# Kernel optimization log

Hardware: AMD Instinct MI355X
Metric: run time of the kernel (lower is better)

Reference implementation:

```python
import jax, jax.numpy as jnp
import numpy as np

N_NODES = 100000
N_EDGES = 3200000
IN_CH, HID, OUT_CH = 11, 64, 1


def setup_inputs() -> dict:
    key = jax.random.key(0)
    ks = jax.random.split(key, 10)
    x = jax.random.normal(ks[0], (N_NODES, IN_CH), dtype=jnp.float32)
    edge_index = jax.random.randint(ks[1], (2, N_EDGES), 0, N_NODES, dtype=jnp.int64)
    s = lambda k, shape, fan_in: jax.random.normal(k, shape, jnp.float32) * (1.0 / np.sqrt(fan_in))
    return {
        "x": x,
        "edge_index": edge_index,
        # conv1: lin_l acts on aggregated neighbors (has bias), lin_r on root (no bias)
        "Wl1": s(ks[2], (HID, IN_CH), IN_CH), "bl1": jnp.zeros((HID,), jnp.float32),
        "Wr1": s(ks[3], (HID, IN_CH), IN_CH),
        "Wl2": s(ks[4], (HID, HID), HID), "bl2": jnp.zeros((HID,), jnp.float32),
        "Wr2": s(ks[5], (HID, HID), HID),
        "Wlin": s(ks[6], (OUT_CH, HID), HID), "blin": jnp.zeros((OUT_CH,), jnp.float32),
    }


def _sage_conv(x, src, dst, Wl, bl, Wr):
    # mean aggregation of source features onto destination nodes
    msg = x[src]                                            # [E, d] gather
    agg = jax.ops.segment_sum(msg, dst, num_segments=N_NODES)          # [N, d]
    cnt = jax.ops.segment_sum(jnp.ones_like(dst, jnp.float32), dst, num_segments=N_NODES)
    mean = agg / jnp.maximum(cnt, 1.0)[:, None]             # isolated nodes -> 0
    return mean @ Wl.T + bl + x @ Wr.T


def reference(x, edge_index, Wl1, bl1, Wr1, Wl2, bl2, Wr2, Wlin, blin):
    src, dst = edge_index[0], edge_index[1]
    h = jax.nn.relu(_sage_conv(x, src, dst, Wl1, bl1, Wr1))
    h = jax.nn.relu(_sage_conv(h, src, dst, Wl2, bl2, Wr2))
    return h @ Wlin.T + blin
```

## Files before the change

kernel.cpp:

```cpp
#include <hip/hip_runtime.h>
#include <hip/hip_fp16.h>

#define IN_CH 11
#define HID 64
#define PAD 64
#define OVCAP 16384
#define NBLK 512
#define BSH 7
#define NBKT 782
#define CAP8 768

typedef _Float16 half8_t __attribute__((ext_vector_type(8)));
typedef float f32x4_t __attribute__((ext_vector_type(4)));

__global__ void k_prep(const float* __restrict__ x, const float* __restrict__ Wl2,
                       const float* __restrict__ Wr2, unsigned* __restrict__ xphu,
                       __half* __restrict__ wl2h, __half* __restrict__ wr2h,
                       int* __restrict__ ovcnt, int* __restrict__ bcnt8, int N) {
    int i = blockIdx.x * blockDim.x + threadIdx.x;
    if (i == 0) *ovcnt = 0;
    if (i < 8 * NBKT) bcnt8[i] = 0;
    if (i < HID * HID) {
        wl2h[i] = __float2half_rn(Wl2[i]);
        wr2h[i] = __float2half_rn(Wr2[i]);
    }
    if (i < (N + 1) * 8) {
        int n = i >> 3, j = (i & 7) * 2;
        float a = 0.f, b = 0.f;
        if (n < N) {
            if (j < IN_CH) a = x[n * IN_CH + j];
            if (j + 1 < IN_CH) b = x[n * IN_CH + j + 1];
        }
        unsigned lo = (unsigned)__half_as_ushort(__float2half_rn(a));
        unsigned hi = (unsigned)__half_as_ushort(__float2half_rn(b));
        xphu[i] = lo | (hi << 16);
    }
}

__global__ __launch_bounds__(256) void k_build(const int* __restrict__ src,
        const int* __restrict__ dst, unsigned* __restrict__ ebuf,
        int* __restrict__ bcnt8, int* __restrict__ ovcnt, int* __restrict__ ov,
        int E, int csz) {
    __shared__ int h[NBKT];
    __shared__ int cur[NBKT];
    __shared__ int lim[NBKT];
    int tid = threadIdx.x, blk = blockIdx.x;
    int xcd = blk & 7;
    for (int t = tid; t < NBKT; t += 256) h[t] = 0;
    __syncthreads();
    int c0 = blk * csz, c1 = min(c0 + csz, E);
    for (int base = c0; base < c1; base += 1024) {
        int d[4]; bool ok[4];
        #pragma unroll
        for (int k = 0; k < 4; k++) {
            int e = base + tid + k * 256;
            ok[k] = e < c1;
            d[k] = ok[k] ? dst[e] : 0;
        }
        #pragma unroll
        for (int k = 0; k < 4; k++)
            if (ok[k]) atomicAdd(&h[d[k] >> BSH], 1);
    }
    __syncthreads();
    for (int t = tid; t < NBKT; t += 256) {
        int hc = h[t];
        int cell = xcd * NBKT + t;
        int base = cell * CAP8;
        int off = (hc > 0) ? atomicAdd(&bcnt8[cell], hc) : 0;
        cur[t] = base + off;
        lim[t] = base + CAP8;
    }
    __syncthreads();
    for (int base = c0; base < c1; base += 1024) {
        int d[4], s[4], slot[4];
        bool ok[4];
        #pragma unroll
        for (int k = 0; k < 4; k++) {
            int e = base + tid + k * 256;
            ok[k] = e < c1;
            d[k] = ok[k] ? dst[e] : 0;
            s[k] = ok[k] ? __builtin_nontemporal_load(&src[e]) : 0;
        }
        #pragma unroll
        for (int k = 0; k < 4; k++)
            if (ok[k]) slot[k] = atomicAdd(&cur[d[k] >> BSH], 1);
        #pragma unroll
        for (int k = 0; k < 4; k++) {
            if (!ok[k]) continue;
            if (slot[k] < lim[d[k] >> BSH]) {
                ebuf[slot[k]] = ((unsigned)s[k] << 7) | (unsigned)(d[k] & 127);
            } else {
                int q = atomicAdd(ovcnt, 1);
                if (q < OVCAP) { ov[2 * q] = d[k]; ov[2 * q + 1] = s[k]; }
            }
        }
    }
}

__global__ __launch_bounds__(256) void k_bbuild(const unsigned* __restrict__ ebuf,
        const int* __restrict__ bcnt8,
        int* __restrict__ cnt, int* __restrict__ col64,
        int* __restrict__ ovcnt, int* __restrict__ ov, int N) {
    __shared__ int lc[128];
    __shared__ int colsh[128 * PAD];
    int tid = threadIdx.x, b = blockIdx.x;
    int lo = b << BSH, hi = min(lo + 128, N);
    #pragma unroll
    for (int i = 0; i < 8; i++)
        ((int4*)colsh)[tid + i * 256] = make_int4(N, N, N, N);
    if (tid < 128) lc[tid] = 0;
    __syncthreads();
    for (int x = 0; x < 8; x++) {
        int cell = x * NBKT + b;
        int cc = min(bcnt8[cell], CAP8);
        const unsigned* seg = ebuf + (size_t)cell * CAP8;
        for (int i = tid; i < cc; i += 256) {
            unsigned p = __builtin_nontemporal_load(&seg[i]);
            int row = (int)(p & 127u);
            int sv  = (int)(p >> 7);
            int r = atomicAdd(&lc[row], 1);
            if (r < PAD) {
                colsh[(row << 6) | r] = sv;
            } else {
                int q = atomicAdd(ovcnt, 1);
                if (q < OVCAP) { ov[2 * q] = lo + row; ov[2 * q + 1] = sv; }
            }
        }
    }
    __syncthreads();
    int nn = hi - lo;
    int4* dst4 = (int4*)col64 + (size_t)lo * 16;
    for (int i = tid; i < nn * 16; i += 256) dst4[i] = ((int4*)colsh)[i];
    if (tid < nn) cnt[lo + tid] = lc[tid];
}

__global__ void k_agg1(const unsigned* __restrict__ xphu,
                       const int* __restrict__ col64,
                       float* __restrict__ agg1, int N) {
    int lane = threadIdx.x & 63;
    int n = blockIdx.x * 4 + (threadIdx.x >> 6);
    if (n >= N) return;
    int c8 = lane & 7, sub = lane >> 3;
    const int* cb = col64 + n * PAD;
    int s[8];
    #pragma unroll
    for (int jj = 0; jj < 8; jj++) s[jj] = __builtin_nontemporal_load(&cb[sub + 8 * jj]);
    unsigned v[8];
    #pragma unroll
    for (int jj = 0; jj < 8; jj++) v[jj] = xphu[s[jj] * 8 + c8];
    __half2 a2 = __floats2half2_rn(0.f, 0.f);
    #pragma unroll
    for (int jj = 0; jj < 8; jj++) a2 = __hadd2(a2, *(__half2*)&v[jj]);
    float2 f = __half22float2(a2);
    #pragma unroll
    for (int off = 8; off <= 32; off <<= 1) {
        f.x += __shfl_xor(f.x, off);
        f.y += __shfl_xor(f.y, off);
    }
    if (lane < 8) ((float2*)agg1)[n * 8 + lane] = f;
}

__global__ void k_ov1(const int* __restrict__ ovcnt, const int* __restrict__ ov,
                      const float* __restrict__ x, float* __restrict__ agg1) {
    int c = *ovcnt; if (c > OVCAP) c = OVCAP;
    for (int i = blockIdx.x * blockDim.x + threadIdx.x; i < c;
         i += gridDim.x * blockDim.x) {
        int d = ov[2 * i], s = ov[2 * i + 1];
        for (int ch = 0; ch < IN_CH; ch++)
            atomicAdd(&agg1[d * 16 + ch], x[s * IN_CH + ch]);
    }
}

__global__ void k_dense1(const float* __restrict__ x, const float* __restrict__ agg1,
                         const int* __restrict__ cnt, const float* __restrict__ Wl,
                         const float* __restrict__ bl, const float* __restrict__ Wr,
                         unsigned* __restrict__ h1h, int N) {
    int lane = threadIdx.x & 63;
    int n = blockIdx.x * 4 + (threadIdx.x >> 6);
    if (n > N) return;
    if (n == N) {
        if (lane < 32) h1h[n * 32 + lane] = 0u;
        return;
    }
    int deg = cnt[n];
    float inv = deg > 0 ? 1.f / (float)deg : 0.f;
    float mv = (lane < 16) ? agg1[n * 16 + lane] * inv : 0.f;
    float xv = (lane < IN_CH) ? x[n * IN_CH + lane] : 0.f;
    float h = bl[lane];
    #pragma unroll
    for (int c = 0; c < IN_CH; c++)
        h += Wl[lane * IN_CH + c] * __shfl(mv, c) + Wr[lane * IN_CH + c] * __shfl(xv, c);
    h = fmaxf(h, 0.f);
    unsigned my = (unsigned)__half_as_ushort(__float2half_rn(h));
    unsigned nx = __shfl_down(my, 1);
    if ((lane & 1) == 0) h1h[n * 32 + (lane >> 1)] = my | (nx << 16);
}

__global__ void k_agg2(const uint4* __restrict__ h1h4, const int* __restrict__ col64,
                       const int* __restrict__ cnt, unsigned* __restrict__ agg2h,
                       int N) {
    int lane = threadIdx.x & 63;
    int n = blockIdx.x * 4 + (threadIdx.x >> 6);
    if (n >= N) return;
    int c8 = lane & 7, sub = lane >> 3;
    const int* cb = col64 + n * PAD;
    int s[8];
    #pragma unroll
    for (int jj = 0; jj < 8; jj++) s[jj] = __builtin_nontemporal_load(&cb[sub + 8 * jj]);
    uint4 v[8];
    #pragma unroll
    for (int jj = 0; jj < 8; jj++) v[jj] = h1h4[s[jj] * 8 + c8];
    __half2 a2[4];
    #pragma unroll
    for (int t = 0; t < 4; t++) a2[t] = __floats2half2_rn(0.f, 0.f);
    #pragma unroll
    for (int jj = 0; jj < 8; jj++) {
        a2[0] = __hadd2(a2[0], *(__half2*)&v[jj].x);
        a2[1] = __hadd2(a2[1], *(__half2*)&v[jj].y);
        a2[2] = __hadd2(a2[2], *(__half2*)&v[jj].z);
        a2[3] = __hadd2(a2[3], *(__half2*)&v[jj].w);
    }
    float acc[8];
    #pragma unroll
    for (int t = 0; t < 4; t++) {
        float2 f = __half22float2(a2[t]);
        acc[2 * t] = f.x; acc[2 * t + 1] = f.y;
    }
    #pragma unroll
    for (int off = 8; off <= 32; off <<= 1) {
        #pragma unroll
        for (int t = 0; t < 8; t++) acc[t] += __shfl_xor(acc[t], off);
    }
    if (sub == 0) {
        int deg = cnt[n];
        float inv = deg > 0 ? 1.f / (float)deg : 0.f;
        __half2 h0 = __floats2half2_rn(acc[0] * inv, acc[1] * inv);
        __half2 h1 = __floats2half2_rn(acc[2] * inv, acc[3] * inv);
        __half2 h2 = __floats2half2_rn(acc[4] * inv, acc[5] * inv);
        __half2 h3 = __floats2half2_rn(acc[6] * inv, acc[7] * inv);
        uint4 o;
        o.x = *(unsigned*)&h0; o.y = *(unsigned*)&h1;
        o.z = *(unsigned*)&h2; o.w = *(unsigned*)&h3;
        ((uint4*)agg2h)[n * 8 + c8] = o;
    }
}

__global__ void k_ov2(const int* __restrict__ ovcnt, const int* __restrict__ ov,
                      const unsigned* __restrict__ h1h, const int* __restrict__ cnt,
                      unsigned* __restrict__ agg2h) {
    int c = *ovcnt; if (c > OVCAP) c = OVCAP;
    for (int i = blockIdx.x * blockDim.x + threadIdx.x; i < c;
         i += gridDim.x * blockDim.x) {
        int d = ov[2 * i], s = ov[2 * i + 1];
        int deg = cnt[d];
        float inv = deg > 0 ? 1.f / (float)deg : 0.f;
        const __half2* hp = (const __half2*)(h1h + s * 32);
        __half2* ap = (__half2*)(agg2h + d * 32);
        for (int ch = 0; ch < 32; ch++) {
            float2 f = __half22float2(hp[ch]);
            __half2 adv = __floats2half2_rn(f.x * inv, f.y * inv);
            unsafeAtomicAdd(&ap[ch], adv);
        }
    }
}

__global__ __launch_bounds__(256) void k_dense2(
    const uint4* __restrict__ agg2h4, const uint4* __restrict__ h1h_u4,
    const __half* __restrict__ wl2h, const __half* __restrict__ wr2h,
    const float* __restrict__ bl, const float* __restrict__ Wlin,
    const float* __restrict__ blin, float* __restrict__ out, int N) {
    union U { uint4 u; half8_t h; };
    int lane = threadIdx.x & 63;
    int wave = blockIdx.x * 4 + (threadIdx.x >> 6);
    int nwaves = gridDim.x * 4;
    int r16 = lane & 15, quad = lane >> 4;
    const uint4* wlu = (const uint4*)wl2h;
    const uint4* wru = (const uint4*)wr2h;
    half8_t bfr[4][4];
    #pragma unroll
    for (int tt = 0; tt < 4; tt++) {
        int o = tt * 16 + r16;
        U t0, t1, t2, t3;
        t0.u = wlu[o * 8 + quad];
        t1.u = wlu[o * 8 + 4 + quad];
        t2.u = wru[o * 8 + quad];
        t3.u = wru[o * 8 + 4 + quad];
        bfr[tt][0] = t0.h; bfr[tt][1] = t1.h; bfr[tt][2] = t2.h; bfr[tt][3] = t3.h;
    }
    float bl_c[4], wl_c[4];
    #pragma unroll
    for (int tt = 0; tt < 4; tt++) {
        bl_c[tt] = bl[tt * 16 + r16];
        wl_c[tt] = Wlin[tt * 16 + r16];
    }
    float b0 = blin[0];
    int ntiles = (N + 15) >> 4;
    for (int t = wave; t < ntiles; t += nwaves) {
        int nb = t * 16;
        int n = nb + r16; if (n >= N) n = N - 1;
        U a0, a1, a2, a3;
        a0.u = agg2h4[n * 8 + quad];
        a1.u = agg2h4[n * 8 + 4 + quad];
        a2.u = h1h_u4[n * 8 + quad];
        a3.u = h1h_u4[n * 8 + 4 + quad];
        float p0 = 0.f, p1 = 0.f, p2 = 0.f, p3 = 0.f;
        #pragma unroll
        for (int tt = 0; tt < 4; tt++) {
            f32x4_t c = {0.f, 0.f, 0.f, 0.f};
            c = __builtin_amdgcn_mfma_f32_16x16x32_f16(a0.h, bfr[tt][0], c, 0, 0, 0);
            c = __builtin_amdgcn_mfma_f32_16x16x32_f16(a1.h, bfr[tt][1], c, 0, 0, 0);
            c = __builtin_amdgcn_mfma_f32_16x16x32_f16(a2.h, bfr[tt][2], c, 0, 0, 0);
            c = __builtin_amdgcn_mfma_f32_16x16x32_f16(a3.h, bfr[tt][3], c, 0, 0, 0);
            p0 += fmaxf(c[0] + bl_c[tt], 0.f) * wl_c[tt];
            p1 += fmaxf(c[1] + bl_c[tt], 0.f) * wl_c[tt];
            p2 += fmaxf(c[2] + bl_c[tt], 0.f) * wl_c[tt];
            p3 += fmaxf(c[3] + bl_c[tt], 0.f) * wl_c[tt];
        }
        #pragma unroll
        for (int off = 1; off <= 8; off <<= 1) {
            p0 += __shfl_xor(p0, off); p1 += __shfl_xor(p1, off);
            p2 += __shfl_xor(p2, off); p3 += __shfl_xor(p3, off);
        }
        if (r16 == 0) {
            int nn = nb + quad * 4;
            if (nn + 3 < N) {
                ((float4*)out)[nn >> 2] = make_float4(p0 + b0, p1 + b0, p2 + b0, p3 + b0);
            } else {
                if (nn + 0 < N) out[nn + 0] = p0 + b0;
                if (nn + 1 < N) out[nn + 1] = p1 + b0;
                if (nn + 2 < N) out[nn + 2] = p2 + b0;
                if (nn + 3 < N) out[nn + 3] = p3 + b0;
            }
        }
    }
}


extern "C" void kernel_launch(void* const* d_in, const int* in_sizes, int n_in,
                              void* d_out, int out_size, void* d_ws, size_t ws_size,
                              hipStream_t stream) {
    const float* x    = (const float*)d_in[0];
    const int*   ei   = (const int*)d_in[1];
    const float* Wl1  = (const float*)d_in[2];
    const float* bl1  = (const float*)d_in[3];
    const float* Wr1  = (const float*)d_in[4];
    const float* Wl2  = (const float*)d_in[5];
    const float* bl2  = (const float*)d_in[6];
    const float* Wr2  = (const float*)d_in[7];
    const float* Wlin = (const float*)d_in[8];
    const float* blin = (const float*)d_in[9];
    float* out = (float*)d_out;

    int N = in_sizes[0] / IN_CH;
    int E = in_sizes[1] / 2;
    const int* srcp = ei;
    const int* dstp = ei + E;

    int* ws       = (int*)d_ws;
    int* cnt      = ws;
    int* ovcnt    = ws + N;
    int* col64    = ws + 100032;
    unsigned* xph = (unsigned*)(ws + 6500032);
    unsigned* ebuf= (unsigned*)(ws + 7300064);
    int* bcnt8    = ws + 12104672;
    float* agg1   = (float*)(ws + 7300064);
    unsigned* agg2h = (unsigned*)(ws + 6500032);
    unsigned* h1h = (unsigned*)(ws + 12900096);
    int* ov       = ws + 16100128;
    __half* wl2h  = (__half*)(ws + 16132896);
    __half* wr2h  = (__half*)(ws + 16134944);

    int csz = (E + NBLK - 1) / NBLK;

    k_prep   <<<((N + 1) * 8 + 255) / 256, 256, 0, stream>>>(x, Wl2, Wr2, xph,
                                                             wl2h, wr2h, ovcnt,
                                                             bcnt8, N);
    k_build  <<<NBLK, 256, 0, stream>>>(srcp, dstp, ebuf, bcnt8, ovcnt, ov, E, csz);
    k_bbuild <<<NBKT, 256, 0, stream>>>(ebuf, bcnt8, cnt, col64, ovcnt, ov, N);

    k_agg1   <<<(N + 3) / 4, 256, 0, stream>>>(xph, col64, agg1, N);
    k_ov1    <<<8, 256, 0, stream>>>(ovcnt, ov, x, agg1);
    k_dense1 <<<(N + 4) / 4, 256, 0, stream>>>(x, agg1, cnt, Wl1, bl1, Wr1, h1h, N);

    k_agg2   <<<(N + 3) / 4, 256, 0, stream>>>((const uint4*)h1h, col64, cnt,
                                               agg2h, N);
    k_ov2    <<<8, 256, 0, stream>>>(ovcnt, ov, h1h, cnt, agg2h);

    k_dense2 <<<512, 256, 0, stream>>>((const uint4*)agg2h, (const uint4*)h1h,
                                       wl2h, wr2h, bl2, Wlin, blin, out, N);
}
```

Measured before the change: 259.9 us.

## Fuse bucket build with layer-1 aggregation and dense, and layer-2 agg with dense

Merges the bucket CSR build, layer-1 neighbor aggregation, overflow handling and layer-1 dense transform into one 512-thread block per 128-node bucket, keeping adjacency and partial sums in shared memory. Layer-2 aggregation, overflow correction and the MFMA dense/output stage are likewise fused per bucket, with weights staged in swizzled LDS. This cuts kernel launches and global round trips for agg1/agg2 buffers. The trade-offs are more shared-memory pressure, lower occupancy, and a serial single-thread overflow scan in each block; overflow entries are tagged with a flag bit so the two overflow sources can be told apart.

Result: no change. 258.0 us (-0.7%).

```diff
diff --git a/kernel.cpp b/kernel.cpp
--- a/kernel.cpp
+++ b/kernel.cpp
@@ -9,6 +9,7 @@
 #define BSH 7
 #define NBKT 782
 #define CAP8 768
+#define OVFLAG (1 << 30)
 
 typedef _Float16 half8_t __attribute__((ext_vector_type(8)));
 typedef float f32x4_t __attribute__((ext_vector_type(4)));
@@ -16,10 +17,12 @@
 __global__ void k_prep(const float* __restrict__ x, const float* __restrict__ Wl2,
                        const float* __restrict__ Wr2, unsigned* __restrict__ xphu,
                        __half* __restrict__ wl2h, __half* __restrict__ wr2h,
-                       int* __restrict__ ovcnt, int* __restrict__ bcnt8, int N) {
+                       int* __restrict__ ovcnt, int* __restrict__ bcnt8,
+                       int* __restrict__ ov, int N) {
     int i = blockIdx.x * blockDim.x + threadIdx.x;
     if (i == 0) *ovcnt = 0;
     if (i < 8 * NBKT) bcnt8[i] = 0;
+    if (i < 2 * OVCAP) ov[i] = 0;
     if (i < HID * HID) {
         wl2h[i] = __float2half_rn(Wl2[i]);
         wr2h[i] = __float2half_rn(Wr2[i]);
@@ -91,30 +94,36 @@
                 ebuf[slot[k]] = ((unsigned)s[k] << 7) | (unsigned)(d[k] & 127);
             } else {
                 int q = atomicAdd(ovcnt, 1);
-                if (q < OVCAP) { ov[2 * q] = d[k]; ov[2 * q + 1] = s[k]; }
+                if (q < OVCAP) { ov[2 * q] = d[k] | OVFLAG; ov[2 * q + 1] = s[k]; }
             }
         }
     }
 }
 
-__global__ __launch_bounds__(256) void k_bbuild(const unsigned* __restrict__ ebuf,
-        const int* __restrict__ bcnt8,
-        int* __restrict__ cnt, int* __restrict__ col64,
-        int* __restrict__ ovcnt, int* __restrict__ ov, int N) {
+__global__ __launch_bounds__(512) void k_fuse1(
+    const unsigned* __restrict__ ebuf, const int* __restrict__ bcnt8,
+    const float* __restrict__ x, const unsigned* __restrict__ xphu,
+    const float* __restrict__ Wl, const float* __restrict__ bl,
+    const float* __restrict__ Wr,
+    int* __restrict__ cnt, int* __restrict__ col64,
+    int* __restrict__ ovcnt, int* __restrict__ ov,
+    unsigned* __restrict__ h1h, int N) {
     __shared__ int lc[128];
     __shared__ int colsh[128 * PAD];
+    __shared__ float aggsh[128][16];
     int tid = threadIdx.x, b = blockIdx.x;
     int lo = b << BSH, hi = min(lo + 128, N);
-    #pragma unroll
-    for (int i = 0; i < 8; i++)
-        ((int4*)colsh)[tid + i * 256] = make_int4(N, N, N, N);
+    int nn = hi - lo;
+    for (int i = tid; i < 128 * PAD / 4; i += 512)
+        ((int4*)colsh)[i] = make_int4(N, N, N, N);
     if (tid < 128) lc[tid] = 0;
-    __syncthreads();
-    for (int x = 0; x < 8; x++) {
-        int cell = x * NBKT + b;
+    for (int i = tid; i < 128 * 16; i += 512) ((float*)aggsh)[i] = 0.f;
+    __syncthreads();
+    for (int xc = 0; xc < 8; xc++) {
+        int cell = xc * NBKT + b;
         int cc = min(bcnt8[cell], CAP8);
         const unsigned* seg = ebuf + (size_t)cell * CAP8;
-        for (int i = tid; i < cc; i += 256) {
+        for (int i = tid; i < cc; i += 512) {
             unsigned p = __builtin_nontemporal_load(&seg[i]);
             int row = (int)(p & 127u);
             int sv  = (int)(p >> 7);
@@ -124,169 +133,175 @@
             } else {
                 int q = atomicAdd(ovcnt, 1);
                 if (q < OVCAP) { ov[2 * q] = lo + row; ov[2 * q + 1] = sv; }
+                for (int ch = 0; ch < IN_CH; ch++)
+                    atomicAdd(&aggsh[row][ch], x[sv * IN_CH + ch]);
             }
         }
     }
     __syncthreads();
-    int nn = hi - lo;
-    int4* dst4 = (int4*)col64 + (size_t)lo * 16;
-    for (int i = tid; i < nn * 16; i += 256) dst4[i] = ((int4*)colsh)[i];
-    if (tid < nn) cnt[lo + tid] = lc[tid];
+    {
+        int c = *ovcnt; if (c > OVCAP) c = OVCAP;
+        for (int i = tid; i < c; i += 512) {
+            int d = ov[2 * i];
+            if (d & OVFLAG) {
+                int dd = d & ~OVFLAG;
+                if (dd >= lo && dd < hi) {
+                    int s = ov[2 * i + 1];
+                    for (int ch = 0; ch < IN_CH; ch++)
+                        atomicAdd(&aggsh[dd - lo][ch], x[s * IN_CH + ch]);
+                }
+            }
+        }
+    }
+    {
+        int4* dst4 = (int4*)col64 + (size_t)lo * 16;
+        for (int i = tid; i < nn * 16; i += 512) dst4[i] = ((int4*)colsh)[i];
+        if (tid < nn) cnt[lo + tid] = lc[tid];
+        if (b == 0 && tid < 32) h1h[(size_t)N * 32 + tid] = 0u;
+    }
+    __syncthreads();
+    int lane = tid & 63, wv = tid >> 6;
+    int c8 = lane & 7, sub = lane >> 3;
+    for (int it = 0; it < 16; it++) {
+        int row = wv * 16 + it;
+        if (row >= nn) continue;
+        int s[8];
+        #pragma unroll
+        for (int jj = 0; jj < 8; jj++) s[jj] = colsh[(row << 6) | (sub + 8 * jj)];
+        unsigned v[8];
+        #pragma unroll
+        for (int jj = 0; jj < 8; jj++) v[jj] = xphu[s[jj] * 8 + c8];
+        __half2 a2 = __floats2half2_rn(0.f, 0.f);
+        #pragma unroll
+        for (int jj = 0; jj < 8; jj++) a2 = __hadd2(a2, *(__half2*)&v[jj]);
+        float2 f = __half22float2(a2);
+        #pragma unroll
+        for (int off = 8; off <= 32; off <<= 1) {
+            f.x += __shfl_xor(f.x, off);
+            f.y += __shfl_xor(f.y, off);
+        }
+        if (lane < 8) {
+            aggsh[row][2 * lane]     += f.x;
+            aggsh[row][2 * lane + 1] += f.y;
+        }
+    }
+    __syncthreads();
+    for (int it = 0; it < 16; it++) {
+        int row = wv * 16 + it;
+        if (row >= nn) continue;
+        int n = lo + row;
+        int deg = lc[row];
+        float inv = deg > 0 ? 1.f / (float)deg : 0.f;
+        float mv = (lane < 16) ? aggsh[row][lane] * inv : 0.f;
+        float xv = (lane < IN_CH) ? x[n * IN_CH + lane] : 0.f;
+        float h = bl[lane];
+        #pragma unroll
+        for (int c = 0; c < IN_CH; c++)
+            h += Wl[lane * IN_CH + c] * __shfl(mv, c) + Wr[lane * IN_CH + c] * __shfl(xv, c);
+        h = fmaxf(h, 0.f);
+        unsigned my = (unsigned)__half_as_ushort(__float2half_rn(h));
+        unsigned nx = __shfl_down(my, 1);
+        if ((lane & 1) == 0) h1h[n * 32 + (lane >> 1)] = my | (nx << 16);
+    }
 }
 
-__global__ void k_agg1(const unsigned* __restrict__ xphu,
-                       const int* __restrict__ col64,
-                       float* __restrict__ agg1, int N) {
-    int lane = threadIdx.x & 63;
-    int n = blockIdx.x * 4 + (threadIdx.x >> 6);
-    if (n >= N) return;
-    int c8 = lane & 7, sub = lane >> 3;
-    const int* cb = col64 + n * PAD;
-    int s[8];
-    #pragma unroll
-    for (int jj = 0; jj < 8; jj++) s[jj] = __builtin_nontemporal_load(&cb[sub + 8 * jj]);
-    unsigned v[8];
-    #pragma unroll
-    for (int jj = 0; jj < 8; jj++) v[jj] = xphu[s[jj] * 8 + c8];
-    __half2 a2 = __floats2half2_rn(0.f, 0.f);
-    #pragma unroll
-    for (int jj = 0; jj < 8; jj++) a2 = __hadd2(a2, *(__half2*)&v[jj]);
-    float2 f = __half22float2(a2);
-    #pragma unroll
-    for (int off = 8; off <= 32; off <<= 1) {
-        f.x += __shfl_xor(f.x, off);
-        f.y += __shfl_xor(f.y, off);
-    }
-    if (lane < 8) ((float2*)agg1)[n * 8 + lane] = f;
-}
-
-__global__ void k_ov1(const int* __restrict__ ovcnt, const int* __restrict__ ov,
-                      const float* __restrict__ x, float* __restrict__ agg1) {
-    int c = *ovcnt; if (c > OVCAP) c = OVCAP;
-    for (int i = blockIdx.x * blockDim.x + threadIdx.x; i < c;
-         i += gridDim.x * blockDim.x) {
-        int d = ov[2 * i], s = ov[2 * i + 1];
-        for (int ch = 0; ch < IN_CH; ch++)
-            atomicAdd(&agg1[d * 16 + ch], x[s * IN_CH + ch]);
-    }
-}
-
-__global__ void k_dense1(const float* __restrict__ x, const float* __restrict__ agg1,
-                         const int* __restrict__ cnt, const float* __restrict__ Wl,
-                         const float* __restrict__ bl, const float* __restrict__ Wr,
-                         unsigned* __restrict__ h1h, int N) {
-    int lane = threadIdx.x & 63;
-    int n = blockIdx.x * 4 + (threadIdx.x >> 6);
-    if (n > N) return;
-    if (n == N) {
-        if (lane < 32) h1h[n * 32 + lane] = 0u;
-        return;
-    }
-    int deg = cnt[n];
-    float inv = deg > 0 ? 1.f / (float)deg : 0.f;
-    float mv = (lane < 16) ? agg1[n * 16 + lane] * inv : 0.f;
-    float xv = (lane < IN_CH) ? x[n * IN_CH + lane] : 0.f;
-    float h = bl[lane];
-    #pragma unroll
-    for (int c = 0; c < IN_CH; c++)
-        h += Wl[lane * IN_CH + c] * __shfl(mv, c) + Wr[lane * IN_CH + c] * __shfl(xv, c);
-    h = fmaxf(h, 0.f);
-    unsigned my = (unsigned)__half_as_ushort(__float2half_rn(h));
-    unsigned nx = __shfl_down(my, 1);
-    if ((lane & 1) == 0) h1h[n * 32 + (lane >> 1)] = my | (nx << 16);
-}
-
-__global__ void k_agg2(const uint4* __restrict__ h1h4, const int* __restrict__ col64,
-                       const int* __restrict__ cnt, unsigned* __restrict__ agg2h,
-                       int N) {
-    int lane = threadIdx.x & 63;
-    int n = blockIdx.x * 4 + (threadIdx.x >> 6);
-    if (n >= N) return;
-    int c8 = lane & 7, sub = lane >> 3;
-    const int* cb = col64 + n * PAD;
-    int s[8];
-    #pragma unroll
-    for (int jj = 0; jj < 8; jj++) s[jj] = __builtin_nontemporal_load(&cb[sub + 8 * jj]);
-    uint4 v[8];
-    #pragma unroll
-    for (int jj = 0; jj < 8; jj++) v[jj] = h1h4[s[jj] * 8 + c8];
-    __half2 a2[4];
-    #pragma unroll
-    for (int t = 0; t < 4; t++) a2[t] = __floats2half2_rn(0.f, 0.f);
-    #pragma unroll
-    for (int jj = 0; jj < 8; jj++) {
-        a2[0] = __hadd2(a2[0], *(__half2*)&v[jj].x);
-        a2[1] = __hadd2(a2[1], *(__half2*)&v[jj].y);
-        a2[2] = __hadd2(a2[2], *(__half2*)&v[jj].z);
-        a2[3] = __hadd2(a2[3], *(__half2*)&v[jj].w);
-    }
-    float acc[8];
-    #pragma unroll
-    for (int t = 0; t < 4; t++) {
-        float2 f = __half22float2(a2[t]);
-        acc[2 * t] = f.x; acc[2 * t + 1] = f.y;
-    }
-    #pragma unroll
-    for (int off = 8; off <= 32; off <<= 1) {
-        #pragma unroll
-        for (int t = 0; t < 8; t++) acc[t] += __shfl_xor(acc[t], off);
-    }
-    if (sub == 0) {
-        int deg = cnt[n];
-        float inv = deg > 0 ? 1.f / (float)deg : 0.f;
-        __half2 h0 = __floats2half2_rn(acc[0] * inv, acc[1] * inv);
-        __half2 h1 = __floats2half2_rn(acc[2] * inv, acc[3] * inv);
-        __half2 h2 = __floats2half2_rn(acc[4] * inv, acc[5] * inv);
-        __half2 h3 = __floats2half2_rn(acc[6] * inv, acc[7] * inv);
-        uint4 o;
-        o.x = *(unsigned*)&h0; o.y = *(unsigned*)&h1;
-        o.z = *(unsigned*)&h2; o.w = *(unsigned*)&h3;
-        ((uint4*)agg2h)[n * 8 + c8] = o;
-    }
-}
-
-__global__ void k_ov2(const int* __restrict__ ovcnt, const int* __restrict__ ov,
-                      const unsigned* __restrict__ h1h, const int* __restrict__ cnt,
-                      unsigned* __restrict__ agg2h) {
-    int c = *ovcnt; if (c > OVCAP) c = OVCAP;
-    for (int i = blockIdx.x * blockDim.x + threadIdx.x; i < c;
-         i += gridDim.x * blockDim.x) {
-        int d = ov[2 * i], s = ov[2 * i + 1];
-        int deg = cnt[d];
-        float inv = deg > 0 ? 1.f / (float)deg : 0.f;
-        const __half2* hp = (const __half2*)(h1h + s * 32);
-        __half2* ap = (__half2*)(agg2h + d * 32);
-        for (int ch = 0; ch < 32; ch++) {
-            float2 f = __half22float2(hp[ch]);
-            __half2 adv = __floats2half2_rn(f.x * inv, f.y * inv);
-            unsafeAtomicAdd(&ap[ch], adv);
-        }
-    }
-}
-
-__global__ __launch_bounds__(256) void k_dense2(
-    const uint4* __restrict__ agg2h4, const uint4* __restrict__ h1h_u4,
+__global__ __launch_bounds__(512) void k_fuse2(
+    const uint4* __restrict__ h1h4, const int* __restrict__ col64,
+    const int* __restrict__ cnt, const int* __restrict__ ovcnt,
+    const int* __restrict__ ov,
     const __half* __restrict__ wl2h, const __half* __restrict__ wr2h,
     const float* __restrict__ bl, const float* __restrict__ Wlin,
     const float* __restrict__ blin, float* __restrict__ out, int N) {
     union U { uint4 u; half8_t h; };
-    int lane = threadIdx.x & 63;
-    int wave = blockIdx.x * 4 + (threadIdx.x >> 6);
-    int nwaves = gridDim.x * 4;
+    __shared__ uint4 meansh[128 * 8];
+    __shared__ uint4 wsh[2][64 * 8];
+    int tid = threadIdx.x, b = blockIdx.x;
+    int lo = b << BSH, hi = min(lo + 128, N);
+    int nn = hi - lo;
+    int lane = tid & 63, wv = tid >> 6;
+    {
+        const uint4* wlu = (const uint4*)wl2h;
+        const uint4* wru = (const uint4*)wr2h;
+        for (int i = tid; i < 64 * 8; i += 512) {
+            int o = i >> 3, q = i & 7;
+            wsh[0][(o << 3) | (q ^ (o & 7))] = wlu[i];
+            wsh[1][(o << 3) | (q ^ (o & 7))] = wru[i];
+        }
+    }
+    int c8 = lane & 7, sub = lane >> 3;
+    for (int it = 0; it < 16; it++) {
+        int row = wv * 16 + it;
+        if (row >= nn) continue;
+        int n = lo + row;
+        const int* cb = col64 + n * PAD;
+        int s[8];
+        #pragma unroll
+        for (int jj = 0; jj < 8; jj++) s[jj] = __builtin_nontemporal_load(&cb[sub + 8 * jj]);
+        uint4 v[8];
+        #pragma unroll
+        for (int jj = 0; jj < 8; jj++) v[jj] = h1h4[s[jj] * 8 + c8];
+        __half2 a2[4];
+        #pragma unroll
+        for (int t = 0; t < 4; t++) a2[t] = __floats2half2_rn(0.f, 0.f);
+        #pragma unroll
+        for (int jj = 0; jj < 8; jj++) {
+            a2[0] = __hadd2(a2[0], *(__half2*)&v[jj].x);
+            a2[1] = __hadd2(a2[1], *(__half2*)&v[jj].y);
+            a2[2] = __hadd2(a2[2], *(__half2*)&v[jj].z);
+            a2[3] = __hadd2(a2[3], *(__half2*)&v[jj].w);
+        }
+        float acc[8];
+        #pragma unroll
+        for (int t = 0; t < 4; t++) {
+            float2 f = __half22float2(a2[t]);
+            acc[2 * t] = f.x; acc[2 * t + 1] = f.y;
+        }
+        #pragma unroll
+        for (int off = 8; off <= 32; off <<= 1) {
+            #pragma unroll
+            for (int t = 0; t < 8; t++) acc[t] += __shfl_xor(acc[t], off);
+        }
+        if (sub == 0) {
+            int deg = cnt[n];
+            float inv = deg > 0 ? 1.f / (float)deg : 0.f;
+            __half2 h0 = __floats2half2_rn(acc[0] * inv, acc[1] * inv);
+            __half2 h1 = __floats2half2_rn(acc[2] * inv, acc[3] * inv);
+            __half2 h2 = __floats2half2_rn(acc[4] * inv, acc[5] * inv);
+            __half2 h3 = __floats2half2_rn(acc[6] * inv, acc[7] * inv);
+            uint4 o;
+            o.x = *(unsigned*)&h0; o.y = *(unsigned*)&h1;
+            o.z = *(unsigned*)&h2; o.w = *(unsigned*)&h3;
+            meansh[(row << 3) | (c8 ^ (row & 7))] = o;
+        }
+    }
+    __syncthreads();
+    if (tid == 0) {
+        int c = *ovcnt; if (c > OVCAP) c = OVCAP;
+        for (int i = 0; i < c; i++) {
+            int d = ov[2 * i] & ~OVFLAG;
+            if (d >= lo && d < hi && (ov[2 * i] != 0)) {
+                int s = ov[2 * i + 1];
+                int row = d - lo;
+                int deg = cnt[d];
+                float inv = deg > 0 ? 1.f / (float)deg : 0.f;
+                for (int q = 0; q < 8; q++) {
+                    uint4* mp = &meansh[(row << 3) | (q ^ (row & 7))];
+                    uint4 m = *mp;
+                    uint4 hh = h1h4[(size_t)s * 8 + q];
+                    __half2* m2 = (__half2*)&m;
+                    __half2* h2v = (__half2*)&hh;
+                    for (int k = 0; k < 4; k++) {
+                        float2 fm = __half22float2(m2[k]);
+                        float2 fh = __half22float2(h2v[k]);
+                        m2[k] = __floats2half2_rn(fm.x + fh.x * inv, fm.y + fh.y * inv);
+                    }
+                    *mp = m;
+                }
+            }
+        }
+    }
+    __syncthreads();
     int r16 = lane & 15, quad = lane >> 4;
-    const uint4* wlu = (const uint4*)wl2h;
-    const uint4* wru = (const uint4*)wr2h;
-    half8_t bfr[4][4];
-    #pragma unroll
-    for (int tt = 0; tt < 4; tt++) {
-        int o = tt * 16 + r16;
-        U t0, t1, t2, t3;
-        t0.u = wlu[o * 8 + quad];
-        t1.u = wlu[o * 8 + 4 + quad];
-        t2.u = wru[o * 8 + quad];
-        t3.u = wru[o * 8 + 4 + quad];
-        bfr[tt][0] = t0.h; bfr[tt][1] = t1.h; bfr[tt][2] = t2.h; bfr[tt][3] = t3.h;
-    }
     float bl_c[4], wl_c[4];
     #pragma unroll
     for (int tt = 0; tt < 4; tt++) {
@@ -294,23 +309,29 @@
         wl_c[tt] = Wlin[tt * 16 + r16];
     }
     float b0 = blin[0];
-    int ntiles = (N + 15) >> 4;
-    for (int t = wave; t < ntiles; t += nwaves) {
-        int nb = t * 16;
-        int n = nb + r16; if (n >= N) n = N - 1;
+    int rb = wv * 16;
+    if (rb < nn) {
+        int row = rb + r16; if (row >= nn) row = nn - 1;
+        int n = lo + row;
         U a0, a1, a2, a3;
-        a0.u = agg2h4[n * 8 + quad];
-        a1.u = agg2h4[n * 8 + 4 + quad];
-        a2.u = h1h_u4[n * 8 + quad];
-        a3.u = h1h_u4[n * 8 + 4 + quad];
+        a0.u = meansh[(row << 3) | (quad ^ (row & 7))];
+        a1.u = meansh[(row << 3) | ((4 + quad) ^ (row & 7))];
+        a2.u = h1h4[(size_t)n * 8 + quad];
+        a3.u = h1h4[(size_t)n * 8 + 4 + quad];
         float p0 = 0.f, p1 = 0.f, p2 = 0.f, p3 = 0.f;
         #pragma unroll
         for (int tt = 0; tt < 4; tt++) {
+            int o = tt * 16 + r16;
+            U b0u, b1u, b2u, b3u;
+            b0u.u = wsh[0][(o << 3) | (quad ^ (o & 7))];
+            b1u.u = wsh[0][(o << 3) | ((4 + quad) ^ (o & 7))];
+            b2u.u = wsh[1][(o << 3) | (quad ^ (o & 7))];
+            b3u.u = wsh[1][(o << 3) | ((4 + quad) ^ (o & 7))];
             f32x4_t c = {0.f, 0.f, 0.f, 0.f};
-            c = __builtin_amdgcn_mfma_f32_16x16x32_f16(a0.h, bfr[tt][0], c, 0, 0, 0);
-            c = __builtin_amdgcn_mfma_f32_16x16x32_f16(a1.h, bfr[tt][1], c, 0, 0, 0);
-            c = __builtin_amdgcn_mfma_f32_16x16x32_f16(a2.h, bfr[tt][2], c, 0, 0, 0);
-            c = __builtin_amdgcn_mfma_f32_16x16x32_f16(a3.h, bfr[tt][3], c, 0, 0, 0);
+            c = __builtin_amdgcn_mfma_f32_16x16x32_f16(a0.h, b0u.h, c, 0, 0, 0);
+            c = __builtin_amdgcn_mfma_f32_16x16x32_f16(a1.h, b1u.h, c, 0, 0, 0);
+            c = __builtin_amdgcn_mfma_f32_16x16x32_f16(a2.h, b2u.h, c, 0, 0, 0);
+            c = __builtin_amdgcn_mfma_f32_16x16x32_f16(a3.h, b3u.h, c, 0, 0, 0);
             p0 += fmaxf(c[0] + bl_c[tt], 0.f) * wl_c[tt];
             p1 += fmaxf(c[1] + bl_c[tt], 0.f) * wl_c[tt];
             p2 += fmaxf(c[2] + bl_c[tt], 0.f) * wl_c[tt];
@@ -322,14 +343,14 @@
             p2 += __shfl_xor(p2, off); p3 += __shfl_xor(p3, off);
         }
         if (r16 == 0) {
-            int nn = nb + quad * 4;
-            if (nn + 3 < N) {
-                ((float4*)out)[nn >> 2] = make_float4(p0 + b0, p1 + b0, p2 + b0, p3 + b0);
+            int nn2 = lo + rb + quad * 4;
+            if (nn2 + 3 < N) {
+                ((float4*)out)[nn2 >> 2] = make_float4(p0 + b0, p1 + b0, p2 + b0, p3 + b0);
             } else {
-                if (nn + 0 < N) out[nn + 0] = p0 + b0;
-                if (nn + 1 < N) out[nn + 1] = p1 + b0;
-                if (nn + 2 < N) out[nn + 2] = p2 + b0;
-                if (nn + 3 < N) out[nn + 3] = p3 + b0;
+                if (nn2 + 0 < N) out[nn2 + 0] = p0 + b0;
+                if (nn2 + 1 < N) out[nn2 + 1] = p1 + b0;
+                if (nn2 + 2 < N) out[nn2 + 2] = p2 + b0;
+                if (nn2 + 3 < N) out[nn2 + 3] = p3 + b0;
             }
         }
     }
@@ -363,8 +384,6 @@
     unsigned* xph = (unsigned*)(ws + 6500032);
     unsigned* ebuf= (unsigned*)(ws + 7300064);
     int* bcnt8    = ws + 12104672;
-    float* agg1   = (float*)(ws + 7300064);
-    unsigned* agg2h = (unsigned*)(ws + 6500032);
     unsigned* h1h = (unsigned*)(ws + 12900096);
     int* ov       = ws + 16100128;
     __half* wl2h  = (__half*)(ws + 16132896);
@@ -372,20 +391,12 @@
 
     int csz = (E + NBLK - 1) / NBLK;
 
-    k_prep   <<<((N + 1) * 8 + 255) / 256, 256, 0, stream>>>(x, Wl2, Wr2, xph,
-                                                             wl2h, wr2h, ovcnt,
-                                                             bcnt8, N);
-    k_build  <<<NBLK, 256, 0, stream>>>(srcp, dstp, ebuf, bcnt8, ovcnt, ov, E, csz);
-    k_bbuild <<<NBKT, 256, 0, stream>>>(ebuf, bcnt8, cnt, col64, ovcnt, ov, N);
-
-    k_agg1   <<<(N + 3) / 4, 256, 0, stream>>>(xph, col64, agg1, N);
-    k_ov1    <<<8, 256, 0, stream>>>(ovcnt, ov, x, agg1);
-    k_dense1 <<<(N + 4) / 4, 256, 0, stream>>>(x, agg1, cnt, Wl1, bl1, Wr1, h1h, N);
-
-    k_agg2   <<<(N + 3) / 4, 256, 0, stream>>>((const uint4*)h1h, col64, cnt,
-                                               agg2h, N);
-    k_ov2    <<<8, 256, 0, stream>>>(ovcnt, ov, h1h, cnt, agg2h);
-
-    k_dense2 <<<512, 256, 0, stream>>>((const uint4*)agg2h, (const uint4*)h1h,
+    k_prep  <<<((N + 1) * 8 + 255) / 256, 256, 0, stream>>>(x, Wl2, Wr2, xph,
+                                                            wl2h, wr2h, ovcnt,
+                                                            bcnt8, ov, N);
+    k_build <<<NBLK, 256, 0, stream>>>(srcp, dstp, ebuf, bcnt8, ovcnt, ov, E, csz);
+    k_fuse1 <<<NBKT, 512, 0, stream>>>(ebuf, bcnt8, x, xph, Wl1, bl1, Wr1,
+                                       cnt, col64, ovcnt, ov, h1h, N);
+    k_fuse2 <<<NBKT, 512, 0, stream>>>((const uint4*)h1h, col64, cnt, ovcnt, ov,
                                        wl2h, wr2h, bl2, Wlin, blin, out, N);
 }
```
